# Optimization experiments

Measured on AMD Instinct MI355X. Metric: run time of the kernel, lower is better.

## Reference

```python
import jax, jax.numpy as jnp
import numpy as np

N_NODES = 50000
N_EDGES = 800000
IN_FEATS = 256
N_HEADS = 4
OUT_FEATS = 32
NEG_SLOPE = 0.2


def setup_inputs() -> dict:
    key = jax.random.key(0)
    k_feat, k_src, k_dst, k_fc, k_al, k_ar, k_res = jax.random.split(key, 7)
    feat = jax.random.normal(k_feat, (N_NODES, IN_FEATS), dtype=jnp.float32)
    src = jax.random.randint(k_src, (N_EDGES,), 0, N_NODES)
    dst = jax.random.randint(k_dst, (N_EDGES,), 0, N_NODES)
    # xavier-normal-ish scales
    s_fc = (2.0 / (IN_FEATS + N_HEADS * OUT_FEATS)) ** 0.5
    W_fc = jax.random.normal(k_fc, (N_HEADS * OUT_FEATS, IN_FEATS), dtype=jnp.float32) * s_fc
    s_a = (2.0 / (1 + N_HEADS * OUT_FEATS)) ** 0.5
    attn_l = jax.random.normal(k_al, (N_HEADS, OUT_FEATS), dtype=jnp.float32) * s_a
    attn_r = jax.random.normal(k_ar, (N_HEADS, OUT_FEATS), dtype=jnp.float32) * s_a
    W_res = jax.random.normal(k_res, (N_HEADS * OUT_FEATS, IN_FEATS), dtype=jnp.float32) * s_fc
    return {"feat": feat, "src": src, "dst": dst, "W_fc": W_fc,
            "attn_l": attn_l, "attn_r": attn_r, "W_res": W_res}


def reference(feat, src, dst, W_fc, attn_l, attn_r, W_res):
    N = feat.shape[0]
    H, D = attn_l.shape
    ones_e = jnp.ones(src.shape[0], dtype=feat.dtype)

    # projection: [N, H, D]
    h = (feat @ W_fc.T).reshape(N, H, D)
    feat_dst = h  # dst features are pre-norm (torch code aliases before * norm)

    # symmetric norm on source side: out_degree^-0.5
    out_deg = jax.ops.segment_sum(ones_e, src, num_segments=N)
    feat_src = h * (jnp.clip(out_deg, 1.0) ** -0.5)[:, None, None]

    # per-node attention halves -> per-edge score, leaky relu
    el = jnp.einsum('nhd,hd->nh', feat_src, attn_l)  # [N, H]
    er = jnp.einsum('nhd,hd->nh', feat_dst, attn_r)  # [N, H]
    e = jax.nn.leaky_relu(el[src] + er[dst], NEG_SLOPE)  # [E, H]

    # edge_softmax over incoming edges of each dst node
    emax = jax.ops.segment_max(e, dst, num_segments=N)
    emax = jnp.where(jnp.isfinite(emax), emax, 0.0)  # guard empty segments
    ex = jnp.exp(e - emax[dst])
    denom = jax.ops.segment_sum(ex, dst, num_segments=N)
    a = ex / denom[dst]  # [E, H]

    # weighted scatter-sum of messages: u_mul_e + sum
    msg = feat_src[src] * a[:, :, None]  # [E, H, D]
    rst = jax.ops.segment_sum(msg, dst, num_segments=N)  # [N, H, D]

    # symmetric norm on destination side: in_degree^0.5
    in_deg = jax.ops.segment_sum(ones_e, dst, num_segments=N)
    rst = rst * jnp.sqrt(jnp.clip(in_deg, 1.0))[:, None, None]

    # residual projection
    rst = rst + (feat @ W_res.T).reshape(N, H, D)
    return rst
```

## Files before the change

kernel.cpp:

```cpp
#include <hip/hip_runtime.h>
#include <hip/hip_bf16.h>
#include <math.h>

#define HD 128
#define IN_F 256
#define NEG_SLOPE 0.2f
#define NMAX 50000
#define GGRID 256
#define CSRC 32

typedef __attribute__((ext_vector_type(8))) short short8;
typedef __attribute__((ext_vector_type(4))) float f32x4;

__device__ __forceinline__ unsigned short f2bf(float x) {
    __hip_bfloat16 b = __float2bfloat16(x);
    return *(unsigned short*)&b;
}
__device__ __forceinline__ float bf2f(unsigned short u) {
    unsigned int v = ((unsigned int)u) << 16;
    float f;
    __builtin_memcpy(&f, &v, 4);
    return f;
}
__device__ __forceinline__ short8 pack8(float4 f0, float4 f1) {
    short8 v;
    v[0] = (short)f2bf(f0.x); v[1] = (short)f2bf(f0.y);
    v[2] = (short)f2bf(f0.z); v[3] = (short)f2bf(f0.w);
    v[4] = (short)f2bf(f1.x); v[5] = (short)f2bf(f1.y);
    v[6] = (short)f2bf(f1.z); v[7] = (short)f2bf(f1.w);
    return v;
}

__global__ __launch_bounds__(1024) void hist_cvt_kernel(
    const int* __restrict__ src, const int* __restrict__ dst,
    unsigned short* __restrict__ pc_src, unsigned short* __restrict__ pc_dst,
    const float4* __restrict__ wfc4, const float4* __restrict__ wres4,
    const float* __restrict__ wfc, const float* __restrict__ attn_l,
    const float* __restrict__ attn_r, ushort4* __restrict__ w16,
    unsigned short* __restrict__ ew16, int n4each,
    int N, int E, int C, int chunk, int chunk_s) {
    __shared__ unsigned int h[NMAX / 2];
    int tid = threadIdx.x;
    int b = blockIdx.x;

    if (b >= C + CSRC) {
        int rb = b - C - CSRC;
        if (rb == 0) {
            int hh = tid >> 8, k = tid & 255;
            float sl = 0.f, sr = 0.f;
#pragma unroll 8
            for (int d = 0; d < 32; d++) {
                float w = wfc[(size_t)(hh * 32 + d) * IN_F + k];
                sl += attn_l[hh * 32 + d] * w;
                sr += attn_r[hh * 32 + d] * w;
            }
            ew16[hh * IN_F + k] = f2bf(sl);
            ew16[(4 + hh) * IN_F + k] = f2bf(sr);
            ew16[(8 + hh) * IN_F + k] = 0;
            ew16[(12 + hh) * IN_F + k] = 0;
        } else {
            int idx = (rb - 1) * 1024 + tid;
            if (idx < 2 * n4each) {
                float4 f = (idx < n4each) ? wfc4[idx] : wres4[idx - n4each];
                ushort4 u;
                u.x = f2bf(f.x); u.y = f2bf(f.y); u.z = f2bf(f.z); u.w = f2bf(f.w);
                w16[idx] = u;
            }
        }
        return;
    }

    int nh = N >> 1;
    uint4* h4 = (uint4*)h;
    for (int i = tid; i < (nh >> 2); i += 1024) h4[i] = make_uint4(0, 0, 0, 0);
    for (int i = (nh & ~3) + tid; i < nh; i += 1024) h[i] = 0;
    __syncthreads();

    bool isSrc = (b >= C);
    const int* arr = isSrc ? src : dst;
    int c = isSrc ? (b - C) : b;
    int ch = isSrc ? chunk_s : chunk;
    int e0 = c * ch, e1 = min(E, (c + 1) * ch);
    for (int e = e0 + tid; e < e1; e += 1024) {
        int v = arr[e];
        atomicAdd(&h[v >> 1], 1u << ((v & 1) << 4));
    }
    __syncthreads();

    unsigned short* pc = (isSrc ? pc_src : pc_dst) + (size_t)c * N;
    uint4* pc4 = (uint4*)pc;
    for (int i = tid; i < (nh >> 2); i += 1024) pc4[i] = h4[i];
    for (int i = (nh & ~3) + tid; i < nh; i += 1024) ((unsigned int*)pc)[i] = h[i];
}

__global__ __launch_bounds__(256) void sum_scan1_kernel(
    const unsigned short* __restrict__ pc_src, unsigned short* __restrict__ pc_dst,
    int* __restrict__ out_cnt, int* __restrict__ deg, int* __restrict__ bsum,
    int N, int C) {
    __shared__ int wsum[4];
    int n = blockIdx.x * 256 + threadIdx.x;
    int sd = 0;
    if (n < N) {
        int ss = 0;
#pragma unroll 4
        for (int c = 0; c < CSRC; c++) ss += pc_src[(size_t)c * N + n];
        for (int c = 0; c < C; c++) {
            unsigned short v = pc_dst[(size_t)c * N + n];
            pc_dst[(size_t)c * N + n] = (unsigned short)sd;
            sd += v;
        }
        out_cnt[n] = ss;
        deg[n] = sd;
    }
    int v = (n < N) ? sd : 0;
#pragma unroll
    for (int d = 1; d < 64; d <<= 1) v += __shfl_xor(v, d);
    if ((threadIdx.x & 63) == 0) wsum[threadIdx.x >> 6] = v;
    __syncthreads();
    if (threadIdx.x == 0) bsum[blockIdx.x] = wsum[0] + wsum[1] + wsum[2] + wsum[3];
}

__global__ __launch_bounds__(256) void scan3_kernel(const int* __restrict__ deg,
                                                    const int* __restrict__ bsum,
                                                    int* __restrict__ row_start,
                                                    int* __restrict__ tilectr,
                                                    int N, int nb, int E) {
    __shared__ int wsum[4];
    __shared__ int sbo[256];
    int tid = threadIdx.x, lane = tid & 63, wid = tid >> 6;
    {
        int v = (tid < nb) ? bsum[tid] : 0;
        int incl = v;
#pragma unroll
        for (int d = 1; d < 64; d <<= 1) {
            int t = __shfl_up(incl, d);
            if (lane >= d) incl += t;
        }
        if (lane == 63) wsum[wid] = incl;
        __syncthreads();
        int woff = 0;
        for (int w = 0; w < wid; w++) woff += wsum[w];
        sbo[tid] = woff + incl - v;
        __syncthreads();
    }
    int boff = sbo[blockIdx.x];
    if (blockIdx.x == 0 && tid == 0) {
        row_start[N] = E;
        *tilectr = 0;
    }
    __syncthreads();

    int i = blockIdx.x * 256 + tid;
    int v = (i < N) ? deg[i] : 0;
    int incl = v;
#pragma unroll
    for (int d = 1; d < 64; d <<= 1) {
        int t = __shfl_up(incl, d);
        if (lane >= d) incl += t;
    }
    if (lane == 63) wsum[wid] = incl;
    __syncthreads();
    int woff = 0;
    for (int w = 0; w < wid; w++) woff += wsum[w];
    int excl = boff + woff + incl - v;
    if (i < N) row_start[i] = excl;
}

__global__ __launch_bounds__(1024, 1) void place_gemm_kernel(
    const int* __restrict__ src, const int* __restrict__ dst,
    const unsigned short* __restrict__ chunkpre, const int* __restrict__ row_start,
    int* __restrict__ esrc,
    const float* __restrict__ feat, const __hip_bfloat16* __restrict__ w16,
    const __hip_bfloat16* __restrict__ ew16, const int* __restrict__ out_cnt,
    unsigned short* __restrict__ h16, unsigned short* __restrict__ resid16,
    float* __restrict__ el, float* __restrict__ er, int* __restrict__ tilectr,
    int N, int E, int C, int chunk, int ntiles) {
    __shared__ __align__(16) char smem[147520];
    int tid = threadIdx.x;

    if ((int)blockIdx.x < C) {
        unsigned int* cur = (unsigned int*)smem;
        int nh = N >> 1;
        const unsigned short* cp = chunkpre + (size_t)blockIdx.x * N;
        const uint4* cp4 = (const uint4*)cp;
        uint4* cur4 = (uint4*)cur;
        for (int i = tid; i < (nh >> 2); i += 1024) cur4[i] = cp4[i];
        for (int i = (nh & ~3) + tid; i < nh; i += 1024)
            cur[i] = ((const unsigned int*)cp)[i];
        __syncthreads();

        int e1 = min(E, (int)(blockIdx.x + 1) * chunk);
        for (int e = blockIdx.x * chunk + tid; e < e1; e += 1024) {
            int d = dst[e], s = src[e];
            int sh = (d & 1) << 4;
            unsigned int old = atomicAdd(&cur[d >> 1], 1u << sh);
            int rank = (old >> sh) & 0xffff;
            esrc[row_start[d] + rank] = s;
        }
        __syncthreads();
    }

    unsigned short* sB = (unsigned short*)smem;
    unsigned short* sA = (unsigned short*)(smem + 131072);
    int* sT = (int*)(smem + 147456);
    int lane = tid & 63, w = tid >> 6;
    int l15 = lane & 15, lg = lane >> 4;
    int c0 = w * 16;
    bool w0 = (w == 0);
    bool isH = (w < 8);
    int colloc = c0 & 127;

#pragma unroll
    for (int it = 0; it < 8; ++it) {
        int idx = it * 1024 + tid;
        int c = idx >> 5, g = idx & 31;
        short8 v = *(const short8*)(w16 + (size_t)c * IN_F + g * 8);
        *(short8*)&sB[c * 256 + ((g ^ (c & 7)) * 8)] = v;
    }
    short8 ereg[8];
    if (w0) {
        const __hip_bfloat16* ep = ew16 + (size_t)l15 * IN_F + lg * 8;
#pragma unroll
        for (int kk = 0; kk < 8; kk++) ereg[kk] = *(const short8*)(ep + kk * 32);
    }

    int srow = tid >> 5, sgc = tid & 31;

    if (tid == 0) *sT = atomicAdd(tilectr, 1);
    __syncthreads();
    int t = *sT;
    float4 fA0, fA1;
    if (t < ntiles) {
        int gm = t * 32 + srow;
        gm = (gm < N) ? gm : (N - 1);
        const float4* fp = (const float4*)(feat + (size_t)gm * IN_F + sgc * 8);
        fA0 = fp[0];
        fA1 = fp[1];
    }

    while (t < ntiles) {
        __syncthreads();
        *(short8*)&sA[srow * 256 + ((sgc ^ (srow & 7)) * 8)] = pack8(fA0, fA1);
        if (tid == 0) *sT = atomicAdd(tilectr, 1);
        __syncthreads();

        int tn = *sT;
        if (tn < ntiles) {
            int gm = tn * 32 + srow;
            gm = (gm < N) ? gm : (N - 1);
            const float4* fp = (const float4*)(feat + (size_t)gm * IN_F + sgc * 8);
            fA0 = fp[0];
            fA1 = fp[1];
        }

        f32x4 acc[2], accE[2];
#pragma unroll
        for (int i = 0; i < 2; i++) {
            acc[i] = (f32x4){0.f, 0.f, 0.f, 0.f};
            accE[i] = (f32x4){0.f, 0.f, 0.f, 0.f};
        }
#pragma unroll
        for (int kk = 0; kk < 8; kk++) {
            short8 a[2], b;
#pragma unroll
            for (int mi = 0; mi < 2; mi++) {
                int row = mi * 16 + l15;
                int gs = (kk * 4 + lg) ^ (row & 7);
                a[mi] = *(const short8*)&sA[row * 256 + gs * 8];
            }
            {
                int c = c0 + l15;
                int gsb = (kk * 4 + lg) ^ (c & 7);
                b = *(const short8*)&sB[c * 256 + gsb * 8];
            }
#pragma unroll
            for (int mi = 0; mi < 2; mi++)
                acc[mi] = __builtin_amdgcn_mfma_f32_16x16x32_bf16(a[mi], b, acc[mi],
                                                                  0, 0, 0);
            if (w0) {
#pragma unroll
                for (int mi = 0; mi < 2; mi++)
                    accE[mi] = __builtin_amdgcn_mfma_f32_16x16x32_bf16(
                        a[mi], ereg[kk], accE[mi], 0, 0, 0);
            }
        }

        int bm = t * 32;
#pragma unroll
        for (int mi = 0; mi < 2; mi++) {
#pragma unroll
            for (int reg = 0; reg < 4; reg++) {
                int r = bm + mi * 16 + lg * 4 + reg;
                bool valid = (r < N);
                int rr = valid ? r : 0;
                if (isH) {
                    float nrm = rsqrtf(fmaxf((float)out_cnt[rr], 1.0f));
                    if (valid) {
                        h16[(size_t)r * HD + colloc + l15] = f2bf(acc[mi][reg] * nrm);
                        if (w0) {
                            float ev = accE[mi][reg];
                            if (l15 < 4) el[r * 4 + l15] = ev * nrm;
                            else if (l15 < 8) er[r * 4 + (l15 - 4)] = ev;
                        }
                    }
                } else if (valid) {
                    resid16[(size_t)r * HD + colloc + l15] = f2bf(acc[mi][reg]);
                }
            }
        }
        t = tn;
    }
}

__global__ __launch_bounds__(256) void agg_kernel(const unsigned short* __restrict__ h16,
                                                  const float* __restrict__ el,
                                                  const float* __restrict__ er,
                                                  const int* __restrict__ row_start,
                                                  const int* __restrict__ esrc,
                                                  const unsigned short* __restrict__ resid16,
                                                  float* __restrict__ out, int N) {
    int wid = threadIdx.x >> 6, lane = threadIdx.x & 63;
    int n = blockIdx.x * 4 + wid;
    if (n >= N) return;
    int es = lane >> 4;
    int l15 = lane & 15;
    int h = l15 >> 2;
    int d0 = l15 * 8;
    int beg = row_start[n], end = row_start[n + 1];
    float erh = er[n * 4 + h];
    float den = 0.f;
    float acc[8];
#pragma unroll
    for (int j = 0; j < 8; j++) acc[j] = 0.f;

    if (beg < end) {
        bool ok0, ok1;
        float ev0, ev1; short8 hv0, hv1;
        {
            int i0 = beg + es, i1 = beg + 4 + es;
            ok0 = i0 < end; ok1 = i1 < end;
            int s0 = esrc[ok0 ? i0 : beg];
            int s1 = esrc[ok1 ? i1 : beg];
            ev0 = el[s0 * 4 + h]; ev1 = el[s1 * 4 + h];
            hv0 = *(const short8*)(h16 + (size_t)s0 * HD + d0);
            hv1 = *(const short8*)(h16 + (size_t)s1 * HD + d0);
        }
        for (int base = beg + 8; base < end; base += 8) {
            int i0 = base + es, i1 = base + 4 + es;
            bool p0 = i0 < end, p1 = i1 < end;
            int t0 = esrc[p0 ? i0 : beg];
            int t1 = esrc[p1 ? i1 : beg];
            float fv0 = el[t0 * 4 + h];
            float fv1 = el[t1 * 4 + h];
            short8 g0 = *(const short8*)(h16 + (size_t)t0 * HD + d0);
            short8 g1 = *(const short8*)(h16 + (size_t)t1 * HD + d0);
            float e0 = ev0 + erh; e0 = (e0 > 0.f) ? e0 : NEG_SLOPE * e0;
            float e1 = ev1 + erh; e1 = (e1 > 0.f) ? e1 : NEG_SLOPE * e1;
            float ex0 = ok0 ? __expf(e0) : 0.f;
            float ex1 = ok1 ? __expf(e1) : 0.f;
            den += ex0 + ex1;
#pragma unroll
            for (int j = 0; j < 8; j++)
                acc[j] += ex0 * bf2f((unsigned short)hv0[j]) +
                          ex1 * bf2f((unsigned short)hv1[j]);
            ok0 = p0; ok1 = p1; ev0 = fv0; ev1 = fv1; hv0 = g0; hv1 = g1;
        }
        float e0 = ev0 + erh; e0 = (e0 > 0.f) ? e0 : NEG_SLOPE * e0;
        float e1 = ev1 + erh; e1 = (e1 > 0.f) ? e1 : NEG_SLOPE * e1;
        float ex0 = ok0 ? __expf(e0) : 0.f;
        float ex1 = ok1 ? __expf(e1) : 0.f;
        den += ex0 + ex1;
#pragma unroll
        for (int j = 0; j < 8; j++)
            acc[j] += ex0 * bf2f((unsigned short)hv0[j]) +
                      ex1 * bf2f((unsigned short)hv1[j]);
    }

#pragma unroll
    for (int m = 16; m < 64; m <<= 1) {
        den += __shfl_xor(den, m);
#pragma unroll
        for (int j = 0; j < 8; j++) acc[j] += __shfl_xor(acc[j], m);
    }

    if (es == 0) {
        const unsigned short* rp = resid16 + (size_t)n * HD + d0;
        short8 rv = *(const short8*)rp;
        int indeg = end - beg;
        float sc = (indeg > 0) ? sqrtf((float)indeg) / den : 0.f;
        float o[8];
#pragma unroll
        for (int j = 0; j < 8; j++)
            o[j] = sc * acc[j] + bf2f((unsigned short)rv[j]);
        float* op = out + (size_t)n * HD + d0;
        *(float4*)op = make_float4(o[0], o[1], o[2], o[3]);
        *(float4*)(op + 4) = make_float4(o[4], o[5], o[6], o[7]);
    }
}

extern "C" void kernel_launch(void* const* d_in, const int* in_sizes, int n_in,
                              void* d_out, int out_size, void* d_ws, size_t ws_size,
                              hipStream_t stream) {
    const float* feat   = (const float*)d_in[0];
    const int*   src    = (const int*)d_in[1];
    const int*   dst    = (const int*)d_in[2];
    const float* W_fc   = (const float*)d_in[3];
    const float* attn_l = (const float*)d_in[4];
    const float* attn_r = (const float*)d_in[5];
    const float* W_res  = (const float*)d_in[6];
    float* out = (float*)d_out;

    int N = in_sizes[0] / IN_F;
    int E = in_sizes[1];
    int nb = (N + 255) / 256;

    size_t off = 0;
    auto alloc = [&](size_t bytes) {
        size_t o = off;
        off = (off + bytes + 255) & ~(size_t)255;
        return o;
    };
    char* ws = (char*)d_ws;
    unsigned short* h16     = (unsigned short*)(ws + alloc((size_t)N * HD * 2));
    unsigned short* resid16 = (unsigned short*)(ws + alloc((size_t)N * HD * 2));
    __hip_bfloat16* w16     = (__hip_bfloat16*)(ws + alloc((size_t)2 * HD * IN_F * 2));
    unsigned short* ew16    = (unsigned short*)(ws + alloc((size_t)16 * IN_F * 2));
    float* el               = (float*)(ws + alloc((size_t)N * 4 * 4));
    float* er               = (float*)(ws + alloc((size_t)N * 4 * 4));
    int* out_cnt            = (int*)(ws + alloc((size_t)N * 4));
    int* deg                = (int*)(ws + alloc((size_t)N * 4));
    int* row_start          = (int*)(ws + alloc((size_t)(N + 1) * 4));
    int* bsum               = (int*)(ws + alloc((size_t)nb * 4));
    int* tilectr            = (int*)(ws + alloc(256));
    int* esrc               = (int*)(ws + alloc((size_t)E * 4));
    unsigned short* pc_src  = (unsigned short*)(ws + alloc((size_t)CSRC * N * 2));

    size_t per_chunk = (size_t)2 * N;
    size_t avail = (ws_size > off + 4096) ? (ws_size - off - 4096) : 0;
    int C = (int)(avail / per_chunk);
    if (C > 128) C = 128;
    if (C < 32) C = 32;
    unsigned short* pc_dst = (unsigned short*)(ws + alloc((size_t)C * N * 2));
    int chunk = (E + C - 1) / C;
    int chunk_s = (E + CSRC - 1) / CSRC;

    int n4each = HD * IN_F / 4;
    int cvtb = (2 * n4each + 1023) / 1024;

    hist_cvt_kernel<<<C + CSRC + 1 + cvtb, 1024, 0, stream>>>(
        src, dst, pc_src, pc_dst,
        (const float4*)W_fc, (const float4*)W_res, W_fc, attn_l, attn_r,
        (ushort4*)w16, ew16, n4each, N, E, C, chunk, chunk_s);

    sum_scan1_kernel<<<nb, 256, 0, stream>>>(pc_src, pc_dst, out_cnt, deg, bsum, N, C);
    scan3_kernel<<<nb, 256, 0, stream>>>(deg, bsum, row_start, tilectr, N, nb, E);

    int ntiles = (N + 31) / 32;
    place_gemm_kernel<<<GGRID, 1024, 0, stream>>>(
        src, dst, pc_dst, row_start, esrc,
        feat, (const __hip_bfloat16*)w16, (const __hip_bfloat16*)ew16, out_cnt,
        h16, resid16, el, er, tilectr, N, E, C, chunk, ntiles);

    int nb4 = (N + 3) / 4;
    agg_kernel<<<nb4, 256, 0, stream>>>(h16, el, er, row_start, esrc, resid16, out, N);
}
```

Baseline: 127.4 us.

## Keep weight fragments in registers and double-buffer A tiles in GEMM loop

Each wave now holds its weight B-fragments in registers rather than staging the whole weight matrix in shared memory, which shrinks LDS use and removes the B reads from LDS. The extra attention-projection matrix moves from wave-0 registers into a small LDS buffer. The A tile becomes double-buffered, with the next tile's atomic fetch and store overlapped, so the loop needs one barrier per tile instead of two. This raises register pressure, and the smaller LDS footprint does not change occupancy at one 1024-thread block per CU.

```diff
diff --git a/kernel.cpp b/kernel.cpp
--- a/kernel.cpp
+++ b/kernel.cpp
@@ -175,7 +175,7 @@
     unsigned short* __restrict__ h16, unsigned short* __restrict__ resid16,
     float* __restrict__ el, float* __restrict__ er, int* __restrict__ tilectr,
     int N, int E, int C, int chunk, int ntiles) {
-    __shared__ __align__(16) char smem[147520];
+    __shared__ __align__(16) char smem[102400];
     int tid = threadIdx.x;
 
     if ((int)blockIdx.x < C) {
@@ -200,9 +200,10 @@
         __syncthreads();
     }
 
-    unsigned short* sB = (unsigned short*)smem;
-    unsigned short* sA = (unsigned short*)(smem + 131072);
-    int* sT = (int*)(smem + 147456);
+    unsigned short* sA0 = (unsigned short*)smem;
+    unsigned short* sA1 = (unsigned short*)(smem + 16384);
+    unsigned short* sE  = (unsigned short*)(smem + 32768);
+    int* sT = (int*)(smem + 40960);
     int lane = tid & 63, w = tid >> 6;
     int l15 = lane & 15, lg = lane >> 4;
     int c0 = w * 16;
@@ -210,25 +211,23 @@
     bool isH = (w < 8);
     int colloc = c0 & 127;
 
-#pragma unroll
-    for (int it = 0; it < 8; ++it) {
-        int idx = it * 1024 + tid;
-        int c = idx >> 5, g = idx & 31;
-        short8 v = *(const short8*)(w16 + (size_t)c * IN_F + g * 8);
-        *(short8*)&sB[c * 256 + ((g ^ (c & 7)) * 8)] = v;
-    }
-    short8 ereg[8];
-    if (w0) {
-        const __hip_bfloat16* ep = ew16 + (size_t)l15 * IN_F + lg * 8;
-#pragma unroll
-        for (int kk = 0; kk < 8; kk++) ereg[kk] = *(const short8*)(ep + kk * 32);
+    short8 breg[8];
+    {
+        const __hip_bfloat16* bp = w16 + (size_t)(c0 + l15) * IN_F + lg * 8;
+#pragma unroll
+        for (int kk = 0; kk < 8; kk++) breg[kk] = *(const short8*)(bp + kk * 32);
+    }
+    if (tid < 512) {
+        int r = tid >> 5, g = tid & 31;
+        short8 v = *(const short8*)(ew16 + r * IN_F + g * 8);
+        *(short8*)&sE[r * 256 + ((g ^ (r & 7)) * 8)] = v;
     }
 
     int srow = tid >> 5, sgc = tid & 31;
 
-    if (tid == 0) *sT = atomicAdd(tilectr, 1);
-    __syncthreads();
-    int t = *sT;
+    if (tid == 0) sT[0] = atomicAdd(tilectr, 1);
+    __syncthreads();
+    int t = sT[0];
     float4 fA0, fA1;
     if (t < ntiles) {
         int gm = t * 32 + srow;
@@ -237,14 +236,16 @@
         fA0 = fp[0];
         fA1 = fp[1];
     }
-
+    if (tid == 0) sT[1] = atomicAdd(tilectr, 1);
+    if (t < ntiles)
+        *(short8*)&sA0[srow * 256 + ((sgc ^ (srow & 7)) * 8)] = pack8(fA0, fA1);
+    __syncthreads();
+
+    int p = 0;
     while (t < ntiles) {
-        __syncthreads();
-        *(short8*)&sA[srow * 256 + ((sgc ^ (srow & 7)) * 8)] = pack8(fA0, fA1);
-        if (tid == 0) *sT = atomicAdd(tilectr, 1);
-        __syncthreads();
-
-        int tn = *sT;
+        unsigned short* sAc = p ? sA1 : sA0;
+        unsigned short* sAn = p ? sA0 : sA1;
+        int tn = sT[p ^ 1];
         if (tn < ntiles) {
             int gm = tn * 32 + srow;
             gm = (gm < N) ? gm : (N - 1);
@@ -252,6 +253,7 @@
             fA0 = fp[0];
             fA1 = fp[1];
         }
+        if (tid == 0) sT[p] = atomicAdd(tilectr, 1);
 
         f32x4 acc[2], accE[2];
 #pragma unroll
@@ -261,27 +263,21 @@
         }
 #pragma unroll
         for (int kk = 0; kk < 8; kk++) {
-            short8 a[2], b;
-#pragma unroll
-            for (int mi = 0; mi < 2; mi++) {
-                int row = mi * 16 + l15;
-                int gs = (kk * 4 + lg) ^ (row & 7);
-                a[mi] = *(const short8*)&sA[row * 256 + gs * 8];
-            }
-            {
-                int c = c0 + l15;
-                int gsb = (kk * 4 + lg) ^ (c & 7);
-                b = *(const short8*)&sB[c * 256 + gsb * 8];
-            }
+            int gs = (kk * 4 + lg) ^ (l15 & 7);
+            short8 a[2];
 #pragma unroll
             for (int mi = 0; mi < 2; mi++)
-                acc[mi] = __builtin_amdgcn_mfma_f32_16x16x32_bf16(a[mi], b, acc[mi],
-                                                                  0, 0, 0);
+                a[mi] = *(const short8*)&sAc[(mi * 16 + l15) * 256 + gs * 8];
+#pragma unroll
+            for (int mi = 0; mi < 2; mi++)
+                acc[mi] = __builtin_amdgcn_mfma_f32_16x16x32_bf16(a[mi], breg[kk],
+                                                                  acc[mi], 0, 0, 0);
             if (w0) {
+                short8 be = *(const short8*)&sE[l15 * 256 + gs * 8];
 #pragma unroll
                 for (int mi = 0; mi < 2; mi++)
                     accE[mi] = __builtin_amdgcn_mfma_f32_16x16x32_bf16(
-                        a[mi], ereg[kk], accE[mi], 0, 0, 0);
+                        a[mi], be, accE[mi], 0, 0, 0);
             }
         }
 
@@ -308,7 +304,12 @@
                 }
             }
         }
+
+        if (tn < ntiles)
+            *(short8*)&sAn[srow * 256 + ((sgc ^ (srow & 7)) * 8)] = pack8(fA0, fA1);
+        __syncthreads();
         t = tn;
+        p ^= 1;
     }
 }
 
```

Result: no change. 128.5 us (+0.9%).
